# Kernel tuning notes

Hardware: AMD Instinct MI355X
Metric: run time of the kernel (lower is better)

Reference implementation:

```python
import jax, jax.numpy as jnp
import numpy as np


def setup_inputs() -> dict:
    key = jax.random.key(0)
    k1, k2 = jax.random.split(key)
    x = jax.random.normal(k1, (32, 56, 56, 256), dtype=jnp.float32)
    conv_w = jax.random.normal(k2, (7, 7, 2, 1), dtype=jnp.float32) * 0.1
    conv_b = jnp.zeros((1,), dtype=jnp.float32)
    return {"x": x, "conv_w": conv_w, "conv_b": conv_b}


def reference(x, conv_w, conv_b):
    # x: [B, H, W, C] (NHWC, as in Keras)
    avg_pool = jnp.mean(x, axis=-1, keepdims=True)          # [B,H,W,1]
    max_pool = jnp.max(x, axis=-1, keepdims=True)           # [B,H,W,1]
    concat = jnp.concatenate([avg_pool, max_pool], axis=-1)  # [B,H,W,2]
    # 7x7 'same' conv, 2 -> 1 channels, HWIO kernel layout
    attn = jax.lax.conv_general_dilated(
        concat, conv_w,
        window_strides=(1, 1), padding='SAME',
        dimension_numbers=('NHWC', 'HWIO', 'NHWC'))
    attn = jax.nn.sigmoid(attn + conv_b)                     # [B,H,W,1]
    return x * attn
```

## Files before the change

kernel.cpp:

```cpp
#include <hip/hip_runtime.h>
#include <math.h>

#define BB 32
#define HH 56
#define WW 56
#define CC 256
#define NPIX (BB * HH * WW)

__global__ __launch_bounds__(256) void pool_kernel(const float* __restrict__ x,
                                                   float* __restrict__ pooled) {
    int wid  = blockIdx.x * 4 + (threadIdx.x >> 6);
    int lane = threadIdx.x & 63;
    const float4* x4 = (const float4*)x;
    size_t base = ((size_t)wid << 8) | (size_t)lane;

    float s[4], m[4];
#pragma unroll
    for (int i = 0; i < 4; ++i) {
        float4 v = x4[base + (size_t)i * 64];
        s[i] = (v.x + v.y) + (v.z + v.w);
        m[i] = fmaxf(fmaxf(v.x, v.y), fmaxf(v.z, v.w));
    }
#pragma unroll
    for (int o = 32; o > 0; o >>= 1) {
#pragma unroll
        for (int i = 0; i < 4; ++i) {
            s[i] += __shfl_down(s[i], o, 64);
            m[i] = fmaxf(m[i], __shfl_down(m[i], o, 64));
        }
    }
    if (lane == 0) {
        float4* p4 = (float4*)pooled;
        p4[wid * 2]     = make_float4(s[0] * (1.0f / 256.0f), m[0],
                                      s[1] * (1.0f / 256.0f), m[1]);
        p4[wid * 2 + 1] = make_float4(s[2] * (1.0f / 256.0f), m[2],
                                      s[3] * (1.0f / 256.0f), m[3]);
    }
}

__global__ __launch_bounds__(256) void fused_kernel(const float* __restrict__ x,
                                                    const float* __restrict__ pooled,
                                                    const float* __restrict__ cw,
                                                    const float* __restrict__ cb,
                                                    float* __restrict__ out) {
    int wid  = blockIdx.x * 4 + (threadIdx.x >> 6);
    int lane = threadIdx.x & 63;

    const float4* x4 = (const float4*)x;
    size_t base = ((size_t)wid << 8) | (size_t)lane;
    float4 v0 = x4[base];
    float4 v1 = x4[base + 64];
    float4 v2 = x4[base + 128];
    float4 v3 = x4[base + 192];

    int g   = lane >> 4;
    int l   = lane & 15;
    int pix = wid * 4 + g;
    int b   = pix / (HH * WW);
    int hw  = pix % (HH * WW);
    int h   = hw / WW;
    int w   = hw % WW;

    const float2* p2 = (const float2*)pooled + (size_t)b * HH * WW;
    const float2* k2 = (const float2*)cw;
    float acc = 0.0f;
#pragma unroll
    for (int t = 0; t < 4; ++t) {
        int tap = l + t * 16;
        if (tap < 49) {
            int dh = tap / 7;
            int dw = tap - dh * 7;
            int ih = h + dh - 3;
            int iw = w + dw - 3;
            if (ih >= 0 && ih < HH && iw >= 0 && iw < WW) {
                float2 p = p2[ih * WW + iw];
                float2 k = k2[tap];
                acc = fmaf(p.y, k.y, fmaf(p.x, k.x, acc));
            }
        }
    }
#pragma unroll
    for (int o = 8; o > 0; o >>= 1) acc += __shfl_xor(acc, o, 64);
    float a = 1.0f / (1.0f + expf(-(acc + cb[0])));

    float a0 = __shfl(a,  0, 64);
    float a1 = __shfl(a, 16, 64);
    float a2 = __shfl(a, 32, 64);
    float a3 = __shfl(a, 48, 64);

    float4* o4 = (float4*)out;
    v0.x *= a0; v0.y *= a0; v0.z *= a0; v0.w *= a0;
    v1.x *= a1; v1.y *= a1; v1.z *= a1; v1.w *= a1;
    v2.x *= a2; v2.y *= a2; v2.z *= a2; v2.w *= a2;
    v3.x *= a3; v3.y *= a3; v3.z *= a3; v3.w *= a3;
    o4[base]       = v0;
    o4[base + 64]  = v1;
    o4[base + 128] = v2;
    o4[base + 192] = v3;
}

extern "C" void kernel_launch(void* const* d_in, const int* in_sizes, int n_in,
                              void* d_out, int out_size, void* d_ws, size_t ws_size,
                              hipStream_t stream) {
    const float* x  = (const float*)d_in[0];
    const float* cw = (const float*)d_in[1];
    const float* cb = (const float*)d_in[2];
    float* out = (float*)d_out;

    float* pooled = (float*)d_ws;

    pool_kernel<<<NPIX / 16, 256, 0, stream>>>(x, pooled);
    fused_kernel<<<NPIX / 16, 256, 0, stream>>>(x, pooled, cw, cb, out);
}
```

Baseline: 195.7 us.

## Merge pooling and conv-scale kernels into one cooperative persistent kernel

Replaces the two-kernel pipeline with a single cooperative kernel launched with a fixed grid of persistent blocks. Each wave grid-strides over pixel groups to compute channel mean/max, then a grid-wide sync separates this from the 7x7 conv, sigmoid and scaling phase. The aim is to remove the inter-kernel launch gap and tail effects. In exchange it adds a grid barrier cost and limits resident waves, which may reduce memory-level parallelism.

```diff
diff --git a/kernel.cpp b/kernel.cpp
--- a/kernel.cpp
+++ b/kernel.cpp
@@ -1,102 +1,108 @@
 #include <hip/hip_runtime.h>
+#include <hip/hip_cooperative_groups.h>
 #include <math.h>
+
+namespace cg = cooperative_groups;
 
 #define BB 32
 #define HH 56
 #define WW 56
 #define CC 256
 #define NPIX (BB * HH * WW)
+#define NTASK (NPIX / 4)
+#define NBLK  1024
+#define NWAVE (NBLK * 4)
 
-__global__ __launch_bounds__(256) void pool_kernel(const float* __restrict__ x,
-                                                   float* __restrict__ pooled) {
-    int wid  = blockIdx.x * 4 + (threadIdx.x >> 6);
-    int lane = threadIdx.x & 63;
+__global__ __launch_bounds__(256, 4) void fused_all(
+    const float* __restrict__ x, const float* __restrict__ cw,
+    const float* __restrict__ cb, float* __restrict__ out,
+    float* __restrict__ pooled)
+{
+    int lane  = threadIdx.x & 63;
+    int wave0 = blockIdx.x * 4 + (threadIdx.x >> 6);
     const float4* x4 = (const float4*)x;
-    size_t base = ((size_t)wid << 8) | (size_t)lane;
 
-    float s[4], m[4];
-#pragma unroll
-    for (int i = 0; i < 4; ++i) {
-        float4 v = x4[base + (size_t)i * 64];
-        s[i] = (v.x + v.y) + (v.z + v.w);
-        m[i] = fmaxf(fmaxf(v.x, v.y), fmaxf(v.z, v.w));
-    }
-#pragma unroll
-    for (int o = 32; o > 0; o >>= 1) {
+    for (int t = wave0; t < NTASK; t += NWAVE) {
+        size_t base = ((size_t)t << 8) | (size_t)lane;
+        float s[4], m[4];
 #pragma unroll
         for (int i = 0; i < 4; ++i) {
-            s[i] += __shfl_down(s[i], o, 64);
-            m[i] = fmaxf(m[i], __shfl_down(m[i], o, 64));
+            float4 v = x4[base + (size_t)i * 64];
+            s[i] = (v.x + v.y) + (v.z + v.w);
+            m[i] = fmaxf(fmaxf(v.x, v.y), fmaxf(v.z, v.w));
+        }
+#pragma unroll
+        for (int o = 32; o > 0; o >>= 1) {
+#pragma unroll
+            for (int i = 0; i < 4; ++i) {
+                s[i] += __shfl_down(s[i], o, 64);
+                m[i] = fmaxf(m[i], __shfl_down(m[i], o, 64));
+            }
+        }
+        if (lane == 0) {
+            float4* p4 = (float4*)pooled;
+            p4[t * 2]     = make_float4(s[0] * (1.0f / 256.0f), m[0],
+                                        s[1] * (1.0f / 256.0f), m[1]);
+            p4[t * 2 + 1] = make_float4(s[2] * (1.0f / 256.0f), m[2],
+                                        s[3] * (1.0f / 256.0f), m[3]);
         }
     }
-    if (lane == 0) {
-        float4* p4 = (float4*)pooled;
-        p4[wid * 2]     = make_float4(s[0] * (1.0f / 256.0f), m[0],
-                                      s[1] * (1.0f / 256.0f), m[1]);
-        p4[wid * 2 + 1] = make_float4(s[2] * (1.0f / 256.0f), m[2],
-                                      s[3] * (1.0f / 256.0f), m[3]);
-    }
-}
 
-__global__ __launch_bounds__(256) void fused_kernel(const float* __restrict__ x,
-                                                    const float* __restrict__ pooled,
-                                                    const float* __restrict__ cw,
-                                                    const float* __restrict__ cb,
-                                                    float* __restrict__ out) {
-    int wid  = blockIdx.x * 4 + (threadIdx.x >> 6);
-    int lane = threadIdx.x & 63;
+    cg::this_grid().sync();
 
-    const float4* x4 = (const float4*)x;
-    size_t base = ((size_t)wid << 8) | (size_t)lane;
-    float4 v0 = x4[base];
-    float4 v1 = x4[base + 64];
-    float4 v2 = x4[base + 128];
-    float4 v3 = x4[base + 192];
+    const float2* k2 = (const float2*)cw;
+    float bias = cb[0];
+    for (int t = wave0; t < NTASK; t += NWAVE) {
+        size_t base = ((size_t)t << 8) | (size_t)lane;
+        float4 v0 = x4[base];
+        float4 v1 = x4[base + 64];
+        float4 v2 = x4[base + 128];
+        float4 v3 = x4[base + 192];
 
-    int g   = lane >> 4;
-    int l   = lane & 15;
-    int pix = wid * 4 + g;
-    int b   = pix / (HH * WW);
-    int hw  = pix % (HH * WW);
-    int h   = hw / WW;
-    int w   = hw % WW;
+        int g   = lane >> 4;
+        int l   = lane & 15;
+        int pix = t * 4 + g;
+        int b   = pix / (HH * WW);
+        int hw  = pix % (HH * WW);
+        int h   = hw / WW;
+        int w   = hw % WW;
 
-    const float2* p2 = (const float2*)pooled + (size_t)b * HH * WW;
-    const float2* k2 = (const float2*)cw;
-    float acc = 0.0f;
+        const float2* p2 = (const float2*)pooled + (size_t)b * HH * WW;
+        float acc = 0.0f;
 #pragma unroll
-    for (int t = 0; t < 4; ++t) {
-        int tap = l + t * 16;
-        if (tap < 49) {
-            int dh = tap / 7;
-            int dw = tap - dh * 7;
-            int ih = h + dh - 3;
-            int iw = w + dw - 3;
-            if (ih >= 0 && ih < HH && iw >= 0 && iw < WW) {
-                float2 p = p2[ih * WW + iw];
-                float2 k = k2[tap];
-                acc = fmaf(p.y, k.y, fmaf(p.x, k.x, acc));
+        for (int tp = 0; tp < 4; ++tp) {
+            int tap = l + tp * 16;
+            if (tap < 49) {
+                int dh = tap / 7;
+                int dw = tap - dh * 7;
+                int ih = h + dh - 3;
+                int iw = w + dw - 3;
+                if (ih >= 0 && ih < HH && iw >= 0 && iw < WW) {
+                    float2 p = p2[ih * WW + iw];
+                    float2 k = k2[tap];
+                    acc = fmaf(p.y, k.y, fmaf(p.x, k.x, acc));
+                }
             }
         }
+#pragma unroll
+        for (int o = 8; o > 0; o >>= 1) acc += __shfl_xor(acc, o, 64);
+        float a = 1.0f / (1.0f + expf(-(acc + bias)));
+
+        float a0 = __shfl(a,  0, 64);
+        float a1 = __shfl(a, 16, 64);
+        float a2 = __shfl(a, 32, 64);
+        float a3 = __shfl(a, 48, 64);
+
+        float4* o4 = (float4*)out;
+        v0.x *= a0; v0.y *= a0; v0.z *= a0; v0.w *= a0;
+        v1.x *= a1; v1.y *= a1; v1.z *= a1; v1.w *= a1;
+        v2.x *= a2; v2.y *= a2; v2.z *= a2; v2.w *= a2;
+        v3.x *= a3; v3.y *= a3; v3.z *= a3; v3.w *= a3;
+        o4[base]       = v0;
+        o4[base + 64]  = v1;
+        o4[base + 128] = v2;
+        o4[base + 192] = v3;
     }
-#pragma unroll
-    for (int o = 8; o > 0; o >>= 1) acc += __shfl_xor(acc, o, 64);
-    float a = 1.0f / (1.0f + expf(-(acc + cb[0])));
-
-    float a0 = __shfl(a,  0, 64);
-    float a1 = __shfl(a, 16, 64);
-    float a2 = __shfl(a, 32, 64);
-    float a3 = __shfl(a, 48, 64);
-
-    float4* o4 = (float4*)out;
-    v0.x *= a0; v0.y *= a0; v0.z *= a0; v0.w *= a0;
-    v1.x *= a1; v1.y *= a1; v1.z *= a1; v1.w *= a1;
-    v2.x *= a2; v2.y *= a2; v2.z *= a2; v2.w *= a2;
-    v3.x *= a3; v3.y *= a3; v3.z *= a3; v3.w *= a3;
-    o4[base]       = v0;
-    o4[base + 64]  = v1;
-    o4[base + 128] = v2;
-    o4[base + 192] = v3;
 }
 
 extern "C" void kernel_launch(void* const* d_in, const int* in_sizes, int n_in,
@@ -106,9 +112,9 @@
     const float* cw = (const float*)d_in[1];
     const float* cb = (const float*)d_in[2];
     float* out = (float*)d_out;
-
     float* pooled = (float*)d_ws;
 
-    pool_kernel<<<NPIX / 16, 256, 0, stream>>>(x, pooled);
-    fused_kernel<<<NPIX / 16, 256, 0, stream>>>(x, pooled, cw, cb, out);
+    void* args[] = {(void*)&x, (void*)&cw, (void*)&cb, (void*)&out, (void*)&pooled};
+    hipLaunchCooperativeKernel((void*)fused_all, dim3(NBLK), dim3(256),
+                               args, 0, stream);
 }
```

Measured after the change: 295.7 us. 1.51x slower.
